# Kernel optimization log

Measured on AMD Instinct MI355X. Metric: run time of the kernel, lower is better.

Reference implementation:

```python
import jax, jax.numpy as jnp
import numpy as np
from jax import lax

B, S, T = 4096, 4096, 2  # batch, seq_length, num_tags (CRF(2) hardcoded in ToNySegmenter)


def setup_inputs() -> dict:
    key = jax.random.key(0)
    k_em, k_st, k_en, k_tr, k_tg, k_len = jax.random.split(key, 6)
    emissions = jax.random.normal(k_em, (B, S, T), dtype=jnp.float32)
    start_transitions = jax.random.uniform(k_st, (T,), dtype=jnp.float32, minval=-1.0, maxval=1.0)
    end_transitions = jax.random.uniform(k_en, (T,), dtype=jnp.float32, minval=-1.0, maxval=1.0)
    transitions = jax.random.uniform(k_tr, (T, T), dtype=jnp.float32, minval=-1.0, maxval=1.0)
    tags = jax.random.randint(k_tg, (B, S), 0, T, dtype=jnp.int64)
    # variable-length sequences; first position always valid (CRF assumes mask[0]==1)
    lengths = jax.random.randint(k_len, (B,), S // 2, S + 1)
    mask = (jnp.arange(S)[None, :] < lengths[:, None]).astype(jnp.int32)
    return {
        'emissions': emissions,
        'start_transitions': start_transitions,
        'end_transitions': end_transitions,
        'transitions': transitions,
        'tags': tags,
        'mask': mask,
    }


def _crf_nll(emissions, start_transitions, end_transitions, transitions, tags, mask):
    # batch_first=True in the torch module -> transpose to time-major (S, B, ...)
    em = jnp.transpose(emissions, (1, 0, 2))      # (S, B, T)
    tg = tags.T                                   # (S, B)
    mk = mask.T.astype(em.dtype)                  # (S, B)
    seq_len, batch = tg.shape

    # ---- numerator: score of the gold path (fully vectorized over time) ----
    emit = jnp.take_along_axis(em, tg[..., None], axis=2)[..., 0]   # (S, B)
    score = start_transitions[tg[0]] + emit[0]                      # (B,)
    trans = transitions[tg[:-1], tg[1:]]                            # (S-1, B)
    score = score + jnp.sum((trans + emit[1:]) * mk[1:], axis=0)
    seq_ends = mk.sum(axis=0).astype(jnp.int32) - 1                 # (B,)
    last_tags = tg[seq_ends, jnp.arange(batch)]
    score = score + end_transitions[last_tags]

    # ---- denominator: forward algorithm via lax.scan over time ----
    init = start_transitions + em[0]                                # (B, T)

    def step(s, x):
        e_i, m_i = x                                                # (B,T), (B,)
        # s[b, prev] + transitions[prev, cur] + e_i[b, cur], logsumexp over prev
        ns = jax.nn.logsumexp(s[:, :, None] + transitions[None, :, :] + e_i[:, None, :], axis=1)
        s = jnp.where(m_i[:, None] > 0, ns, s)
        return s, None

    final, _ = lax.scan(step, init, (em[1:], mk[1:]))
    normalizer = jax.nn.logsumexp(final + end_transitions, axis=1)  # (B,)

    return -(score - normalizer).mean()


def reference(emissions, start_transitions, end_transitions, transitions, tags, mask):
    return _crf_nll(emissions, start_transitions, end_transitions, transitions, tags, mask)
```

## Files before the change

kernel.cpp:

```cpp
#include <hip/hip_runtime.h>

#define B_CONST 4096
#define S_CONST 4096

#define NEGBIG (-1e30f)

__device__ __forceinline__ float lse2(float a, float b) {
    float m = fmaxf(a, b);
    float d = fminf(a, b) - m;
    return m + __logf(1.0f + __expf(d));
}

struct Seg { float m00, m01, m10, m11; };

__device__ __forceinline__ Seg seg_compose(const Seg& L, const Seg& R) {
    Seg o;
    o.m00 = lse2(L.m00 + R.m00, L.m01 + R.m10);
    o.m01 = lse2(L.m00 + R.m01, L.m01 + R.m11);
    o.m10 = lse2(L.m10 + R.m00, L.m11 + R.m10);
    o.m11 = lse2(L.m10 + R.m01, L.m11 + R.m11);
    return o;
}

__global__ __launch_bounds__(256) void crf_lens_kernel(
    const int* __restrict__ mask, int* __restrict__ lens)
{
    const int lane = threadIdx.x & 63;
    const int wid  = threadIdx.x >> 6;
    const int b    = blockIdx.x * 4 + wid;
    if (b >= B_CONST) return;
    const int* mk = mask + (size_t)b * S_CONST;

    int v1 = mk[lane * 64];
    unsigned long long bal1 = __ballot(v1);
    int nb = __popcll(bal1);
    int base = (nb - 1) * 64;
    int v2 = mk[base + lane];
    unsigned long long bal2 = __ballot(v2);
    int L = base + __popcll(bal2);
    if (lane == 0) lens[b] = L;
}

__global__ __launch_bounds__(1024) void crf_row_kernel(
    const float* __restrict__ em,
    const float* __restrict__ st,
    const float* __restrict__ en,
    const float* __restrict__ tr,
    const int*   __restrict__ tags,
    const int*   __restrict__ lens,
    float* __restrict__ out)
{
    const int b   = blockIdx.x;
    const int tid = threadIdx.x;
    const int lane = tid & 63, wid = tid >> 6;
    const float* em_row = em   + (size_t)b * S_CONST * 2;
    const int*   tg_row = tags + (size_t)b * S_CONST;

    const int L = lens[b];

    const float t00 = tr[0], t01 = tr[1], t10 = tr[2], t11 = tr[3];

    const int c0   = tid * 4;
    const int myHi = min(c0 + 4, L);
    const bool active = (c0 < L);

    Seg seg; seg.m00 = 0.0f; seg.m11 = 0.0f; seg.m01 = NEGBIG; seg.m10 = NEGBIG;
    float sc = 0.0f;

    int4 tg4 = make_int4(0, 0, 0, 0);
    if (active) tg4 = *(const int4*)(tg_row + c0);

    int prev = __shfl_up(tg4.w, 1);
    if (lane == 0) prev = (c0 > 0 && active) ? tg_row[c0 - 1] : 0;

    if (active) {
        const float4* emv = (const float4*)(em_row + 2 * c0);
        float4 eA = emv[0];
        float4 eB = emv[1];

        #define STEP(T_, E0_, E1_, TG_)                                      \
            do {                                                             \
                int t_ = (T_);                                               \
                if (t_ >= 1 && t_ < myHi) {                                  \
                    float e0_ = (E0_), e1_ = (E1_);                          \
                    Seg M;                                                   \
                    M.m00 = t00 + e0_; M.m01 = t01 + e1_;                    \
                    M.m10 = t10 + e0_; M.m11 = t11 + e1_;                    \
                    seg = seg_compose(seg, M);                               \
                    float trv = prev ? ((TG_) ? t11 : t10)                   \
                                     : ((TG_) ? t01 : t00);                  \
                    sc += trv + ((TG_) ? e1_ : e0_);                         \
                }                                                            \
                prev = (TG_);                                                \
            } while (0)

        STEP(c0 + 0, eA.x, eA.y, tg4.x);
        STEP(c0 + 1, eA.z, eA.w, tg4.y);
        STEP(c0 + 2, eB.x, eB.y, tg4.z);
        STEP(c0 + 3, eB.z, eB.w, tg4.w);
        #undef STEP
    }

    #pragma unroll
    for (int s = 1; s < 64; s <<= 1) {
        Seg r;
        r.m00 = __shfl_down(seg.m00, s);
        r.m01 = __shfl_down(seg.m01, s);
        r.m10 = __shfl_down(seg.m10, s);
        r.m11 = __shfl_down(seg.m11, s);
        float rsc = __shfl_down(sc, s);
        seg = seg_compose(seg, r);
        sc += rsc;
    }

    __shared__ Seg   wseg[16];
    __shared__ float wsc[16];
    if (lane == 0) { wseg[wid] = seg; wsc[wid] = sc; }
    __syncthreads();

    if (tid == 0) {
        Seg P = wseg[0];
        float scT = wsc[0];
        #pragma unroll
        for (int w = 1; w < 16; ++w) { P = seg_compose(P, wseg[w]); scT += wsc[w]; }

        float e00 = em_row[0], e01 = em_row[1];
        float st0 = st[0], st1 = st[1];
        float en0 = en[0], en1 = en[1];

        float i0 = st0 + e00, i1 = st1 + e01;
        float f0 = lse2(i0 + P.m00, i1 + P.m10);
        float f1 = lse2(i0 + P.m01, i1 + P.m11);
        float norm = lse2(f0 + en0, f1 + en1);

        int tg0 = tg_row[0];
        int tgL = tg_row[L - 1];
        float score = (tg0 ? st1 : st0) + (tg0 ? e01 : e00) + scT
                    + (tgL ? en1 : en0);

        atomicAdd(out, (norm - score) * (1.0f / (float)B_CONST));
    }
}

extern "C" void kernel_launch(void* const* d_in, const int* in_sizes, int n_in,
                              void* d_out, int out_size, void* d_ws, size_t ws_size,
                              hipStream_t stream) {
    const float* em   = (const float*)d_in[0];
    const float* st   = (const float*)d_in[1];
    const float* en   = (const float*)d_in[2];
    const float* tr   = (const float*)d_in[3];
    const int*   tags = (const int*)d_in[4];
    const int*   mask = (const int*)d_in[5];

    int*   lens = (int*)d_ws;
    float* out  = (float*)d_out;

    hipMemsetAsync(out, 0, sizeof(float) * out_size, stream);
    crf_lens_kernel<<<(B_CONST + 3) / 4, 256, 0, stream>>>(mask, lens);
    crf_row_kernel<<<B_CONST, 1024, 0, stream>>>(em, st, en, tr, tags, lens, out);
}
```

Measured before the change: 324.3 us.

## Fuse length computation into row kernel and restructure block reduction via LDS

Drops the separate lengths kernel: every wave in each block now finds the sequence length itself with two ballot reads of the mask, which removes one launch and the workspace round trip. The per-thread segment starts from the first transition matrix instead of composing with identity, saving one compose. The block reduction changes from a full 64-lane shuffle tree in every wave plus a serial 16-way compose to a single write of all segments to swizzled LDS, 16-element serial composes by 64 threads, then one wave shuffle tree. This cuts shuffle and compose work for most waves, at the cost of more LDS traffic and redundant mask reads in every wave.

Measured after the change: 290.6 us. -10.4%, faster.

```diff
diff --git a/kernel.cpp b/kernel.cpp
--- a/kernel.cpp
+++ b/kernel.cpp
@@ -22,24 +22,7 @@
     return o;
 }
 
-__global__ __launch_bounds__(256) void crf_lens_kernel(
-    const int* __restrict__ mask, int* __restrict__ lens)
-{
-    const int lane = threadIdx.x & 63;
-    const int wid  = threadIdx.x >> 6;
-    const int b    = blockIdx.x * 4 + wid;
-    if (b >= B_CONST) return;
-    const int* mk = mask + (size_t)b * S_CONST;
-
-    int v1 = mk[lane * 64];
-    unsigned long long bal1 = __ballot(v1);
-    int nb = __popcll(bal1);
-    int base = (nb - 1) * 64;
-    int v2 = mk[base + lane];
-    unsigned long long bal2 = __ballot(v2);
-    int L = base + __popcll(bal2);
-    if (lane == 0) lens[b] = L;
-}
+__device__ __forceinline__ int swz(int s) { return s ^ ((s >> 4) & 15); }
 
 __global__ __launch_bounds__(1024) void crf_row_kernel(
     const float* __restrict__ em,
@@ -47,22 +30,29 @@
     const float* __restrict__ en,
     const float* __restrict__ tr,
     const int*   __restrict__ tags,
-    const int*   __restrict__ lens,
+    const int*   __restrict__ mask,
     float* __restrict__ out)
 {
-    const int b   = blockIdx.x;
-    const int tid = threadIdx.x;
-    const int lane = tid & 63, wid = tid >> 6;
+    const int b    = blockIdx.x;
+    const int tid  = threadIdx.x;
+    const int lane = tid & 63;
+
     const float* em_row = em   + (size_t)b * S_CONST * 2;
     const int*   tg_row = tags + (size_t)b * S_CONST;
+    const int*   mk     = mask + (size_t)b * S_CONST;
 
-    const int L = lens[b];
+    int v1 = mk[lane << 6];
+    unsigned long long bal1 = __ballot(v1 != 0);
+    int base = (__popcll(bal1) - 1) << 6;
+    int v2 = mk[base + lane];
+    const int L = base + __popcll(__ballot(v2 != 0));
 
     const float t00 = tr[0], t01 = tr[1], t10 = tr[2], t11 = tr[3];
 
-    const int c0   = tid * 4;
-    const int myHi = min(c0 + 4, L);
+    const int  c0     = tid * 4;
+    const int  myHi   = min(c0 + 4, L);
     const bool active = (c0 < L);
+    const int  lo     = (c0 == 0) ? 1 : c0;
 
     Seg seg; seg.m00 = 0.0f; seg.m11 = 0.0f; seg.m01 = NEGBIG; seg.m10 = NEGBIG;
     float sc = 0.0f;
@@ -86,7 +76,8 @@
                     Seg M;                                                   \
                     M.m00 = t00 + e0_; M.m01 = t01 + e1_;                    \
                     M.m10 = t10 + e0_; M.m11 = t11 + e1_;                    \
-                    seg = seg_compose(seg, M);                               \
+                    if (t_ == lo) seg = M;                                   \
+                    else          seg = seg_compose(seg, M);                 \
                     float trv = prev ? ((TG_) ? t11 : t10)                   \
                                      : ((TG_) ? t01 : t00);                  \
                     sc += trv + ((TG_) ? e1_ : e0_);                         \
@@ -101,44 +92,56 @@
         #undef STEP
     }
 
-    #pragma unroll
-    for (int s = 1; s < 64; s <<= 1) {
-        Seg r;
-        r.m00 = __shfl_down(seg.m00, s);
-        r.m01 = __shfl_down(seg.m01, s);
-        r.m10 = __shfl_down(seg.m10, s);
-        r.m11 = __shfl_down(seg.m11, s);
-        float rsc = __shfl_down(sc, s);
-        seg = seg_compose(seg, r);
-        sc += rsc;
-    }
-
-    __shared__ Seg   wseg[16];
-    __shared__ float wsc[16];
-    if (lane == 0) { wseg[wid] = seg; wsc[wid] = sc; }
+    __shared__ float4 ssegs[1024];
+    __shared__ float  sscs[1024];
+    const int ph = swz(tid);
+    ssegs[ph] = make_float4(seg.m00, seg.m01, seg.m10, seg.m11);
+    sscs[ph]  = sc;
     __syncthreads();
 
-    if (tid == 0) {
-        Seg P = wseg[0];
-        float scT = wsc[0];
+    if (tid < 64) {
+        const int s0 = tid << 4;
+        float4 v = ssegs[swz(s0)];
+        Seg P; P.m00 = v.x; P.m01 = v.y; P.m10 = v.z; P.m11 = v.w;
+        float scT = sscs[swz(s0)];
         #pragma unroll
-        for (int w = 1; w < 16; ++w) { P = seg_compose(P, wseg[w]); scT += wsc[w]; }
+        for (int k = 1; k < 16; ++k) {
+            const int p = swz(s0 + k);
+            float4 r4 = ssegs[p];
+            Seg R; R.m00 = r4.x; R.m01 = r4.y; R.m10 = r4.z; R.m11 = r4.w;
+            P = seg_compose(P, R);
+            scT += sscs[p];
+        }
 
-        float e00 = em_row[0], e01 = em_row[1];
-        float st0 = st[0], st1 = st[1];
-        float en0 = en[0], en1 = en[1];
+        #pragma unroll
+        for (int s = 1; s < 64; s <<= 1) {
+            Seg r;
+            r.m00 = __shfl_down(P.m00, s);
+            r.m01 = __shfl_down(P.m01, s);
+            r.m10 = __shfl_down(P.m10, s);
+            r.m11 = __shfl_down(P.m11, s);
+            float rsc = __shfl_down(scT, s);
+            P = seg_compose(P, r);
+            scT += rsc;
+        }
 
-        float i0 = st0 + e00, i1 = st1 + e01;
-        float f0 = lse2(i0 + P.m00, i1 + P.m10);
-        float f1 = lse2(i0 + P.m01, i1 + P.m11);
-        float norm = lse2(f0 + en0, f1 + en1);
+        if (tid == 0) {
+            float e00 = em_row[0], e01 = em_row[1];
+            float st0 = st[0], st1 = st[1];
+            float en0 = en[0], en1 = en[1];
 
-        int tg0 = tg_row[0];
-        int tgL = tg_row[L - 1];
-        float score = (tg0 ? st1 : st0) + (tg0 ? e01 : e00) + scT
-                    + (tgL ? en1 : en0);
+            float i0 = st0 + e00, i1 = st1 + e01;
+            float f0 = lse2(i0 + P.m00, i1 + P.m10);
+            float f1 = lse2(i0 + P.m01, i1 + P.m11);
+            float norm = lse2(f0 + en0, f1 + en1);
 
-        atomicAdd(out, (norm - score) * (1.0f / (float)B_CONST));
+            int tg0 = tg_row[0];
+            int tgL = tg_row[L - 1];
+            float score = (tg0 ? st1 : st0) + (tg0 ? e01 : e00) + scT
+                        + (tgL ? en1 : en0);
+
+            atomicAdd(out, (norm - score) * (1.0f / (float)B_CONST));
+        }
     }
 }
 
@@ -152,10 +155,8 @@
     const int*   tags = (const int*)d_in[4];
     const int*   mask = (const int*)d_in[5];
 
-    int*   lens = (int*)d_ws;
-    float* out  = (float*)d_out;
+    float* out = (float*)d_out;
 
     hipMemsetAsync(out, 0, sizeof(float) * out_size, stream);
-    crf_lens_kernel<<<(B_CONST + 3) / 4, 256, 0, stream>>>(mask, lens);
-    crf_row_kernel<<<B_CONST, 1024, 0, stream>>>(em, st, en, tr, tags, lens, out);
+    crf_row_kernel<<<B_CONST, 1024, 0, stream>>>(em, st, en, tr, tags, mask, out);
 }
```

## Split CRF row scan into per-wave partial kernel plus batched final combine

Applied to the files above, without the earlier changes.

Each row now runs on 256 threads, and each thread handles 16 timesteps instead of 4. The per-wave segment matrices and gold-path scores are written to workspace, and the old shared-memory block reduction with a single thread finalising each row is removed. A new final kernel combines the four wave segments per row, one thread per row, and reduces the NLL with wave shuffles before the atomic add, so there are far fewer atomics. The log-sum-exp now works in base 2 (exp2/log2 with pre-scaled inputs), and the first timestep seeds the segment directly instead of composing with the identity. The cost is an extra kernel launch and a workspace round trip.

After: 289.5 us. 1.12x faster.

```diff
diff --git a/kernel.cpp b/kernel.cpp
--- a/kernel.cpp
+++ b/kernel.cpp
@@ -4,21 +4,23 @@
 #define S_CONST 4096
 
 #define NEGBIG (-1e30f)
-
-__device__ __forceinline__ float lse2(float a, float b) {
+#define LOG2E  1.44269504088896340736f
+#define LN2    0.69314718055994530942f
+
+__device__ __forceinline__ float lse2b(float a, float b) {
     float m = fmaxf(a, b);
     float d = fminf(a, b) - m;
-    return m + __logf(1.0f + __expf(d));
+    return m + __log2f(1.0f + exp2f(d));
 }
 
 struct Seg { float m00, m01, m10, m11; };
 
 __device__ __forceinline__ Seg seg_compose(const Seg& L, const Seg& R) {
     Seg o;
-    o.m00 = lse2(L.m00 + R.m00, L.m01 + R.m10);
-    o.m01 = lse2(L.m00 + R.m01, L.m01 + R.m11);
-    o.m10 = lse2(L.m10 + R.m00, L.m11 + R.m10);
-    o.m11 = lse2(L.m10 + R.m01, L.m11 + R.m11);
+    o.m00 = lse2b(L.m00 + R.m00, L.m01 + R.m10);
+    o.m01 = lse2b(L.m00 + R.m01, L.m01 + R.m11);
+    o.m10 = lse2b(L.m10 + R.m00, L.m11 + R.m10);
+    o.m11 = lse2b(L.m10 + R.m01, L.m11 + R.m11);
     return o;
 }
 
@@ -30,63 +32,64 @@
     const int b    = blockIdx.x * 4 + wid;
     if (b >= B_CONST) return;
     const int* mk = mask + (size_t)b * S_CONST;
-
-    int v1 = mk[lane * 64];
-    unsigned long long bal1 = __ballot(v1);
-    int nb = __popcll(bal1);
-    int base = (nb - 1) * 64;
+    int v1 = mk[lane << 6];
+    unsigned long long bal1 = __ballot(v1 != 0);
+    int base = (__popcll(bal1) - 1) << 6;
     int v2 = mk[base + lane];
-    unsigned long long bal2 = __ballot(v2);
-    int L = base + __popcll(bal2);
-    if (lane == 0) lens[b] = L;
-}
-
-__global__ __launch_bounds__(1024) void crf_row_kernel(
+    if (lane == 0) lens[b] = base + __popcll(__ballot(v2 != 0));
+}
+
+__global__ __launch_bounds__(256) void crf_scan_kernel(
     const float* __restrict__ em,
-    const float* __restrict__ st,
-    const float* __restrict__ en,
     const float* __restrict__ tr,
     const int*   __restrict__ tags,
     const int*   __restrict__ lens,
-    float* __restrict__ out)
+    float4*      __restrict__ wsegs,
+    float*       __restrict__ wscs)
 {
-    const int b   = blockIdx.x;
-    const int tid = threadIdx.x;
-    const int lane = tid & 63, wid = tid >> 6;
+    const int b    = blockIdx.x;
+    const int wid  = threadIdx.x >> 6;
+    const int lane = threadIdx.x & 63;
+    const int cb   = wid << 10;
+    const int c0   = cb + (lane << 4);
+
     const float* em_row = em   + (size_t)b * S_CONST * 2;
     const int*   tg_row = tags + (size_t)b * S_CONST;
-
-    const int L = lens[b];
+    const int    L      = lens[b];
 
     const float t00 = tr[0], t01 = tr[1], t10 = tr[2], t11 = tr[3];
-
-    const int c0   = tid * 4;
-    const int myHi = min(c0 + 4, L);
+    const float s00 = t00 * LOG2E, s01 = t01 * LOG2E;
+    const float s10 = t10 * LOG2E, s11 = t11 * LOG2E;
+
+    const int  myHi   = min(c0 + 16, L);
     const bool active = (c0 < L);
+    const int  lo     = (c0 == 0) ? 1 : c0;
 
     Seg seg; seg.m00 = 0.0f; seg.m11 = 0.0f; seg.m01 = NEGBIG; seg.m10 = NEGBIG;
     float sc = 0.0f;
 
-    int4 tg4 = make_int4(0, 0, 0, 0);
-    if (active) tg4 = *(const int4*)(tg_row + c0);
-
-    int prev = __shfl_up(tg4.w, 1);
-    if (lane == 0) prev = (c0 > 0 && active) ? tg_row[c0 - 1] : 0;
-
+    int4 tgq[4] = {{0,0,0,0},{0,0,0,0},{0,0,0,0},{0,0,0,0}};
     if (active) {
-        const float4* emv = (const float4*)(em_row + 2 * c0);
-        float4 eA = emv[0];
-        float4 eB = emv[1];
+        const int4* tv = (const int4*)(tg_row + c0);
+        tgq[0] = tv[0]; tgq[1] = tv[1]; tgq[2] = tv[2]; tgq[3] = tv[3];
+    }
+    int prev = __shfl_up(tgq[3].w, 1);
+    if (lane == 0) prev = (cb > 0) ? tg_row[cb - 1] : 0;
+
+    if (active) {
+        const float4* ev = (const float4*)(em_row + 2 * c0);
 
         #define STEP(T_, E0_, E1_, TG_)                                      \
             do {                                                             \
                 int t_ = (T_);                                               \
                 if (t_ >= 1 && t_ < myHi) {                                  \
                     float e0_ = (E0_), e1_ = (E1_);                          \
+                    float e0s = e0_ * LOG2E, e1s = e1_ * LOG2E;              \
                     Seg M;                                                   \
-                    M.m00 = t00 + e0_; M.m01 = t01 + e1_;                    \
-                    M.m10 = t10 + e0_; M.m11 = t11 + e1_;                    \
-                    seg = seg_compose(seg, M);                               \
+                    M.m00 = s00 + e0s; M.m01 = s01 + e1s;                    \
+                    M.m10 = s10 + e0s; M.m11 = s11 + e1s;                    \
+                    if (t_ == lo) seg = M;                                   \
+                    else          seg = seg_compose(seg, M);                 \
                     float trv = prev ? ((TG_) ? t11 : t10)                   \
                                      : ((TG_) ? t01 : t00);                  \
                     sc += trv + ((TG_) ? e1_ : e0_);                         \
@@ -94,10 +97,19 @@
                 prev = (TG_);                                                \
             } while (0)
 
-        STEP(c0 + 0, eA.x, eA.y, tg4.x);
-        STEP(c0 + 1, eA.z, eA.w, tg4.y);
-        STEP(c0 + 2, eB.x, eB.y, tg4.z);
-        STEP(c0 + 3, eB.z, eB.w, tg4.w);
+        #pragma unroll
+        for (int g = 0; g < 4; ++g) {
+            const int tb = c0 + 4 * g;
+            if (tb < myHi) {
+                float4 eA = ev[2 * g];
+                float4 eB = ev[2 * g + 1];
+                int4   t4 = tgq[g];
+                STEP(tb + 0, eA.x, eA.y, t4.x);
+                STEP(tb + 1, eA.z, eA.w, t4.y);
+                STEP(tb + 2, eB.x, eB.y, t4.z);
+                STEP(tb + 3, eB.z, eB.w, t4.w);
+            }
+        }
         #undef STEP
     }
 
@@ -113,33 +125,58 @@
         sc += rsc;
     }
 
-    __shared__ Seg   wseg[16];
-    __shared__ float wsc[16];
-    if (lane == 0) { wseg[wid] = seg; wsc[wid] = sc; }
-    __syncthreads();
-
-    if (tid == 0) {
-        Seg P = wseg[0];
-        float scT = wsc[0];
-        #pragma unroll
-        for (int w = 1; w < 16; ++w) { P = seg_compose(P, wseg[w]); scT += wsc[w]; }
-
-        float e00 = em_row[0], e01 = em_row[1];
-        float st0 = st[0], st1 = st[1];
-        float en0 = en[0], en1 = en[1];
-
-        float i0 = st0 + e00, i1 = st1 + e01;
-        float f0 = lse2(i0 + P.m00, i1 + P.m10);
-        float f1 = lse2(i0 + P.m01, i1 + P.m11);
-        float norm = lse2(f0 + en0, f1 + en1);
-
-        int tg0 = tg_row[0];
-        int tgL = tg_row[L - 1];
-        float score = (tg0 ? st1 : st0) + (tg0 ? e01 : e00) + scT
-                    + (tgL ? en1 : en0);
-
-        atomicAdd(out, (norm - score) * (1.0f / (float)B_CONST));
-    }
+    if (lane == 0) {
+        wsegs[b * 4 + wid] = make_float4(seg.m00, seg.m01, seg.m10, seg.m11);
+        wscs [b * 4 + wid] = sc;
+    }
+}
+
+__global__ __launch_bounds__(256) void crf_final_kernel(
+    const float* __restrict__ em,
+    const float* __restrict__ st,
+    const float* __restrict__ en,
+    const int*   __restrict__ tags,
+    const int*   __restrict__ lens,
+    const float4* __restrict__ wsegs,
+    const float* __restrict__ wscs,
+    float* __restrict__ out)
+{
+    const int r = blockIdx.x * 256 + threadIdx.x;
+
+    float4 v = wsegs[r * 4];
+    Seg P; P.m00 = v.x; P.m01 = v.y; P.m10 = v.z; P.m11 = v.w;
+    float scT = wscs[r * 4];
+    #pragma unroll
+    for (int w = 1; w < 4; ++w) {
+        float4 rv = wsegs[r * 4 + w];
+        Seg R; R.m00 = rv.x; R.m01 = rv.y; R.m10 = rv.z; R.m11 = rv.w;
+        P = seg_compose(P, R);
+        scT += wscs[r * 4 + w];
+    }
+
+    const float* em_row = em   + (size_t)r * S_CONST * 2;
+    const int*   tg_row = tags + (size_t)r * S_CONST;
+    const int    L      = lens[r];
+
+    float e00 = em_row[0], e01 = em_row[1];
+    float st0 = st[0], st1 = st[1];
+    float en0 = en[0], en1 = en[1];
+
+    float i0 = (st0 + e00) * LOG2E, i1 = (st1 + e01) * LOG2E;
+    float f0 = lse2b(i0 + P.m00, i1 + P.m10);
+    float f1 = lse2b(i0 + P.m01, i1 + P.m11);
+    float norm = lse2b(f0 + en0 * LOG2E, f1 + en1 * LOG2E) * LN2;
+
+    int tg0 = tg_row[0];
+    int tgL = tg_row[L - 1];
+    float score = (tg0 ? st1 : st0) + (tg0 ? e01 : e00) + scT
+                + (tgL ? en1 : en0);
+
+    float nll = norm - score;
+
+    #pragma unroll
+    for (int d = 32; d >= 1; d >>= 1) nll += __shfl_down(nll, d);
+    if ((threadIdx.x & 63) == 0) atomicAdd(out, nll * (1.0f / (float)B_CONST));
 }
 
 extern "C" void kernel_launch(void* const* d_in, const int* in_sizes, int n_in,
@@ -152,10 +189,14 @@
     const int*   tags = (const int*)d_in[4];
     const int*   mask = (const int*)d_in[5];
 
-    int*   lens = (int*)d_ws;
-    float* out  = (float*)d_out;
+    float4* wsegs = (float4*)d_ws;
+    float*  wscs  = (float*)((char*)d_ws + (size_t)B_CONST * 4 * sizeof(float4));
+    int*    lens  = (int*)((char*)wscs + (size_t)B_CONST * 4 * sizeof(float));
+
+    float* out = (float*)d_out;
 
     hipMemsetAsync(out, 0, sizeof(float) * out_size, stream);
     crf_lens_kernel<<<(B_CONST + 3) / 4, 256, 0, stream>>>(mask, lens);
-    crf_row_kernel<<<B_CONST, 1024, 0, stream>>>(em, st, en, tr, tags, lens, out);
-}
+    crf_scan_kernel<<<B_CONST, 256, 0, stream>>>(em, tr, tags, lens, wsegs, wscs);
+    crf_final_kernel<<<B_CONST / 256, 256, 0, stream>>>(em, st, en, tags, lens, wsegs, wscs, out);
+}
```
